# Performance work log

Hardware: AMD Instinct MI355X
Metric: run time of the kernel (lower is better)

## Reference

```python
import jax, jax.numpy as jnp
import numpy as np

N = 25000      # nodes
E = 400000     # edges
IN = 1024      # in_channels
FC = 128       # feature_channels
ADD = 20       # additional_channels
MID = (FC + ADD) // 4   # 37, fc1 output (heads=4)
OUT = 3
EPS = 1e-5
NEG_SLOPE = 0.01


def setup_inputs() -> dict:
    key = jax.random.key(0)
    ks = jax.random.split(key, 16)
    d = {}
    d["features"] = jax.random.normal(ks[0], (N, IN), dtype=jnp.float32)
    d["edges"] = jax.random.randint(ks[1], (2, E), 0, N, dtype=jnp.int64)
    d["edges2"] = jax.random.randint(ks[2], (2, 1000), 0, N, dtype=jnp.int64)
    d["edge_features"] = jax.random.normal(ks[3], (E, 1), dtype=jnp.float32)
    d["additional_feature"] = jax.random.normal(ks[4], (N, ADD), dtype=jnp.float32)
    # SAGEConv params: lin_l (neighbor path, with bias), lin_r (root path, no bias)
    s = 1.0 / np.sqrt(IN)
    d["Wl"] = jax.random.uniform(ks[5], (FC, IN), jnp.float32, -s, s)
    d["bl"] = jax.random.uniform(ks[6], (FC,), jnp.float32, -s, s)
    d["Wr"] = jax.random.uniform(ks[7], (FC, IN), jnp.float32, -s, s)
    s1 = 1.0 / np.sqrt(FC + ADD)
    d["W1"] = jax.random.uniform(ks[8], (MID, FC + ADD), jnp.float32, -s1, s1)
    d["b1"] = jax.random.uniform(ks[9], (MID,), jnp.float32, -s1, s1)
    s2 = 1.0 / np.sqrt(MID)
    d["W2"] = jax.random.uniform(ks[10], (OUT, MID), jnp.float32, -s2, s2)
    d["b2"] = jax.random.uniform(ks[11], (OUT,), jnp.float32, -s2, s2)
    # BatchNorm1d (eval mode -> running stats)
    d["gamma"] = jnp.ones((MID,), jnp.float32)
    d["beta"] = jnp.zeros((MID,), jnp.float32)
    d["run_mean"] = jax.random.normal(ks[12], (MID,), dtype=jnp.float32) * 0.1
    d["run_var"] = jnp.abs(jax.random.normal(ks[13], (MID,), dtype=jnp.float32)) * 0.1 + 1.0
    return d


def reference(features, edges, edges2, edge_features, additional_feature,
              Wl, bl, Wr, W1, b1, W2, b2, gamma, beta, run_mean, run_var):
    src, dst = edges[0], edges[1]  # PyG: messages flow source -> target
    # scatter-mean of neighbor features onto targets
    agg = jax.ops.segment_sum(features[src], dst, num_segments=N)        # [N, IN]
    deg = jax.ops.segment_sum(jnp.ones((E,), features.dtype), dst, num_segments=N)
    agg = agg / jnp.maximum(deg, 1.0)[:, None]
    # SAGEConv: lin_l(mean_neigh) + lin_r(x)
    x = agg @ Wl.T + bl + features @ Wr.T                                 # [N, FC]
    x = jnp.where(x >= 0, x, NEG_SLOPE * x)                               # leaky_relu
    # dropout is identity in eval mode
    x = jnp.concatenate([x, additional_feature], axis=1) @ W1.T + b1      # [N, MID]
    x = jnp.maximum(x, 0.0)                                               # relu
    x = gamma * (x - run_mean) * jax.lax.rsqrt(run_var + EPS) + beta      # BN eval
    return x @ W2.T + b2                                                  # [N, OUT]
```

## Files before the change

### kernel.cpp

```cpp
#include <hip/hip_runtime.h>

#define N_NODES 25000
#define N_EDGES 400000
#define IN_CH 1024
#define FC 128
#define ADD_CH 20
#define XCH 148
#define MID 37
#define OUT_CH 3
#define MAXDEG 64
#define CSTRIDE 16

typedef short bf16x8 __attribute__((ext_vector_type(8)));
typedef float f32x4 __attribute__((ext_vector_type(4)));

__device__ __forceinline__ float bflo(unsigned int v) {
    return __builtin_bit_cast(float, v << 16);
}
__device__ __forceinline__ float bfhi(unsigned int v) {
    return __builtin_bit_cast(float, v & 0xffff0000u);
}
__device__ __forceinline__ unsigned int cvtpk(float a, float b) {
    unsigned int r;
    asm("v_cvt_pk_bf16_f32 %0, %1, %2" : "=v"(r) : "v"(a), "v"(b));
    return r;
}

__device__ __forceinline__ void gload16(const void* g, void* l) {
    __builtin_amdgcn_global_load_lds(
        (const __attribute__((address_space(1))) unsigned int*)g,
        (__attribute__((address_space(3))) unsigned int*)l,
        16, 0, 0);
}

#define WSWZ_B 16
#define ZERO_B 49

__global__ __launch_bounds__(512) void prep(const float* __restrict__ Wl,
                                            const float* __restrict__ Wr,
                                            ushort* __restrict__ Wpk,
                                            int* __restrict__ cursor) {
    int b = blockIdx.x, t = threadIdx.x;
    if (b < WSWZ_B) {
        int w = t >> 6, lane = t & 63, l15 = lane & 15, q8 = (lane >> 4) * 8;
        int ch = b * 16 + l15;
        const float* src = (ch < FC) ? (Wl + (size_t)ch * IN_CH)
                                     : (Wr + (size_t)(ch - FC) * IN_CH);
        #pragma unroll
        for (int j = 0; j < 4; ++j) {
            int kt = w * 4 + j;
            float4 lo = *(const float4*)(src + kt * 32 + q8);
            float4 hi = *(const float4*)(src + kt * 32 + q8 + 4);
            uint4 pk;
            pk.x = cvtpk(lo.x, lo.y); pk.y = cvtpk(lo.z, lo.w);
            pk.z = cvtpk(hi.x, hi.y); pk.w = cvtpk(hi.z, hi.w);
            ((uint4*)Wpk)[((size_t)kt * 16 + b) * 64 + lane] = pk;
        }
    } else {
        int i = (b - WSWZ_B) * 512 + t;
        if (i < N_NODES) {
            uint4 z = {0, 0, 0, 0};
            uint4* dst = (uint4*)(cursor + (size_t)i * CSTRIDE);
            dst[0] = z; dst[1] = z; dst[2] = z; dst[3] = z;
        }
    }
}

#define GEMM_B 391
#define BUILD_B 196

__global__ __launch_bounds__(512, 4) void gemm_build(const float* __restrict__ A,
                                                     const ushort* __restrict__ Wpk,
                                                     ushort* __restrict__ Py,
                                                     ushort* __restrict__ Pz,
                                                     const int* __restrict__ edges,
                                                     int* __restrict__ cursor,
                                                     int* __restrict__ col) {
    __shared__ uint4 LDS[3][1536];
    int b = blockIdx.x, t = threadIdx.x;
    if (b >= GEMM_B) {
        int base = (b - GEMM_B) * 2048 + t;
        int src[4], dst[4], pos[4];
        #pragma unroll
        for (int k = 0; k < 4; ++k) {
            int e = base + k * 512;
            bool v = (e < N_EDGES);
            dst[k] = v ? edges[N_EDGES + e] : 0;
            src[k] = v ? edges[e] : 0;
        }
        #pragma unroll
        for (int k = 0; k < 4; ++k) {
            int e = base + k * 512;
            if (e < N_EDGES)
                pos[k] = atomicAdd(&cursor[(size_t)dst[k] * CSTRIDE], 1);
        }
        #pragma unroll
        for (int k = 0; k < 4; ++k) {
            int e = base + k * 512;
            if (e < N_EDGES && pos[k] < MAXDEG)
                col[dst[k] * MAXDEG + pos[k]] = src[k];
        }
        return;
    }
    int m0 = b * 64;

    int ga = t >> 7, hq = (t >> 6) & 1, la = t & 63;
    int nodeA = m0 + ga * 16 + (la & 15);
    if (nodeA >= N_NODES) nodeA = N_NODES - 1;
    const float* Asrc = A + (size_t)nodeA * IN_CH + (la >> 4) * 8 + hq * 4;
    const uint4* Wg = (const uint4*)Wpk;
    int tb = t & ~63;

    int w = t >> 6, lane = t & 63;
    int wm = w >> 2, wn = w & 3;
    int l15 = lane & 15, q = lane >> 4;

    f32x4 acc[4][2] = {};

    gload16(Wg + t,        &LDS[0][tb]);
    gload16(Wg + 512 + t,  &LDS[0][512 + tb]);
    gload16(Asrc,          &LDS[0][1024 + tb]);
    gload16(Wg + 1024 + t,       &LDS[1][tb]);
    gload16(Wg + 1024 + 512 + t, &LDS[1][512 + tb]);
    gload16(Asrc + 32,           &LDS[1][1024 + tb]);

    #define COMPUTE(bc)                                                           \
    {                                                                             \
        bf16x8 wf[4];                                                             \
        _Pragma("unroll")                                                         \
        for (int i = 0; i < 4; ++i)                                               \
            wf[i] = *(const bf16x8*)&LDS[bc][(wn * 4 + i) * 64 + lane];           \
        bf16x8 af[2];                                                             \
        _Pragma("unroll")                                                         \
        for (int g2 = 0; g2 < 2; ++g2) {                                          \
            f32x4 lo = *(const f32x4*)&LDS[bc][1024 + ((wm * 2 + g2) * 2 + 0) * 64 + lane]; \
            f32x4 hi = *(const f32x4*)&LDS[bc][1024 + ((wm * 2 + g2) * 2 + 1) * 64 + lane]; \
            uint4 pk;                                                             \
            pk.x = cvtpk(lo[0], lo[1]); pk.y = cvtpk(lo[2], lo[3]);               \
            pk.z = cvtpk(hi[0], hi[1]); pk.w = cvtpk(hi[2], hi[3]);               \
            af[g2] = __builtin_bit_cast(bf16x8, pk);                              \
        }                                                                         \
        _Pragma("unroll")                                                         \
        for (int i = 0; i < 4; ++i)                                               \
            _Pragma("unroll")                                                     \
            for (int g2 = 0; g2 < 2; ++g2)                                        \
                acc[i][g2] = __builtin_amdgcn_mfma_f32_16x16x32_bf16(wf[i], af[g2], acc[i][g2], 0, 0, 0); \
    }

    int bc = 0, bs = 2;
    for (int c = 0; c < 30; ++c) {
        const uint4* ws = Wg + (size_t)(c + 2) * 1024;
        gload16(ws + t,       &LDS[bs][tb]);
        gload16(ws + 512 + t, &LDS[bs][512 + tb]);
        gload16(Asrc + (size_t)(c + 2) * 32, &LDS[bs][1024 + tb]);
        asm volatile("s_waitcnt vmcnt(6)" ::: "memory");
        __builtin_amdgcn_sched_barrier(0);
        __builtin_amdgcn_s_barrier();
        __builtin_amdgcn_sched_barrier(0);
        COMPUTE(bc);
        __builtin_amdgcn_s_barrier();
        __builtin_amdgcn_sched_barrier(0);
        bc = (bc == 2) ? 0 : bc + 1;
        bs = (bs == 2) ? 0 : bs + 1;
    }
    asm volatile("s_waitcnt vmcnt(3)" ::: "memory");
    __builtin_amdgcn_sched_barrier(0);
    __builtin_amdgcn_s_barrier();
    __builtin_amdgcn_sched_barrier(0);
    COMPUTE(bc);
    bc = (bc == 2) ? 0 : bc + 1;
    asm volatile("s_waitcnt vmcnt(0)" ::: "memory");
    __builtin_amdgcn_sched_barrier(0);
    __builtin_amdgcn_s_barrier();
    __builtin_amdgcn_sched_barrier(0);
    COMPUTE(bc);
    #undef COMPUTE

    #pragma unroll
    for (int g2 = 0; g2 < 2; ++g2) {
        int node = m0 + wm * 32 + g2 * 16 + l15;
        if (node < N_NODES) {
            ushort* base = (wn < 2) ? (Py + (size_t)node * FC + (wn & 1) * 64 + q * 4)
                                    : (Pz + (size_t)node * FC + (wn & 1) * 64 + q * 4);
            #pragma unroll
            for (int i = 0; i < 4; ++i) {
                f32x4 v = acc[i][g2];
                uint2 pk;
                pk.x = cvtpk(v[0], v[1]);
                pk.y = cvtpk(v[2], v[3]);
                *(uint2*)(base + i * 16) = pk;
            }
        }
    }
}

__global__ __launch_bounds__(512) void fused_tail(const ushort* __restrict__ Py,
                                                  const ushort* __restrict__ Pz,
                                                  const int* __restrict__ deg,
                                                  const int* __restrict__ col,
                                                  const float* __restrict__ addf,
                                                  const float* __restrict__ bl,
                                                  const float* __restrict__ W1,
                                                  const float* __restrict__ b1,
                                                  const float* __restrict__ W2,
                                                  const float* __restrict__ b2,
                                                  const float* __restrict__ gamma,
                                                  const float* __restrict__ beta,
                                                  const float* __restrict__ rmean,
                                                  const float* __restrict__ rvar,
                                                  float* __restrict__ out) {
    __shared__ float W1s[XCH][MID + 3];
    __shared__ float xbuf[32][XCH + 4];
    __shared__ float hbuf[32][MID + 3];
    int t = threadIdx.x;
    for (int idx = t; idx < MID * XCH; idx += 512) {
        int j = idx / XCH, k = idx - j * XCH;
        W1s[k][j] = W1[idx];
    }
    __syncthreads();
    int w = t >> 6, lane = t & 63;
    int g = lane >> 4, c16 = lane & 15;
    #pragma unroll 1
    for (int i4 = 0; i4 < 4; ++i4) {
        int sidx = w * 4 + i4;
        int n = blockIdx.x * 32 + sidx;
        bool valid = (n < N_NODES);
        int d = valid ? deg[(size_t)n * CSTRIDE] : 0;
        if (d > MAXDEG) d = MAXDEG;
        float s[8] = {0.f, 0.f, 0.f, 0.f, 0.f, 0.f, 0.f, 0.f};
        if (d > 0) {
            int cidx = col[n * MAXDEG + (lane < d ? lane : 0)];
            for (int i = 0; i < d; i += 16) {
                int e[4];
                uint4 v[4];
                #pragma unroll
                for (int j = 0; j < 4; ++j) {
                    int ee = i + g + j * 4;
                    e[j] = __shfl(cidx, (ee < d) ? ee : 0);
                }
                #pragma unroll
                for (int j = 0; j < 4; ++j)
                    v[j] = *(const uint4*)&Py[(size_t)e[j] * FC + c16 * 8];
                #pragma unroll
                for (int j = 0; j < 4; ++j) {
                    if (i + g + j * 4 < d) {
                        s[0] += bflo(v[j].x); s[1] += bfhi(v[j].x);
                        s[2] += bflo(v[j].y); s[3] += bfhi(v[j].y);
                        s[4] += bflo(v[j].z); s[5] += bfhi(v[j].z);
                        s[6] += bflo(v[j].w); s[7] += bfhi(v[j].w);
                    }
                }
            }
            #pragma unroll
            for (int r = 0; r < 8; ++r) {
                s[r] += __shfl_xor(s[r], 16);
                s[r] += __shfl_xor(s[r], 32);
            }
        }
        if (valid) {
            if (lane < 16) {
                #pragma unroll
                for (int r = 0; r < 8; ++r) xbuf[sidx][lane * 8 + r] = s[r];
            }
            float invd = 1.0f / (float)(d > 1 ? d : 1);
            unsigned int vr = *(const unsigned int*)&Pz[(size_t)n * FC + lane * 2];
            float x0 = xbuf[sidx][2 * lane] * invd + bl[2 * lane] + bflo(vr);
            float x1 = xbuf[sidx][2 * lane + 1] * invd + bl[2 * lane + 1] + bfhi(vr);
            x0 = (x0 >= 0.f) ? x0 : 0.01f * x0;
            x1 = (x1 >= 0.f) ? x1 : 0.01f * x1;
            xbuf[sidx][2 * lane] = x0;
            xbuf[sidx][2 * lane + 1] = x1;
            if (lane < ADD_CH) xbuf[sidx][FC + lane] = addf[(size_t)n * ADD_CH + lane];
            if (lane < MID) {
                float h = b1[lane];
                #pragma unroll 4
                for (int k = 0; k < XCH; ++k) h += W1s[k][lane] * xbuf[sidx][k];
                h = fmaxf(h, 0.0f);
                h = gamma[lane] * (h - rmean[lane]) * rsqrtf(rvar[lane] + 1e-5f) + beta[lane];
                hbuf[sidx][lane] = h;
            }
            if (lane < OUT_CH) {
                float o = b2[lane];
                #pragma unroll
                for (int j = 0; j < MID; ++j) o += W2[lane * MID + j] * hbuf[sidx][j];
                out[(size_t)n * OUT_CH + lane] = o;
            }
        }
    }
}


extern "C" void kernel_launch(void* const* d_in, const int* in_sizes, int n_in,
                              void* d_out, int out_size, void* d_ws, size_t ws_size,
                              hipStream_t stream) {
    const float* features = (const float*)d_in[0];
    const int*   edges    = (const int*)d_in[1];
    const float* addf     = (const float*)d_in[4];
    const float* Wl       = (const float*)d_in[5];
    const float* bl       = (const float*)d_in[6];
    const float* Wr       = (const float*)d_in[7];
    const float* W1       = (const float*)d_in[8];
    const float* b1       = (const float*)d_in[9];
    const float* W2       = (const float*)d_in[10];
    const float* b2       = (const float*)d_in[11];
    const float* gamma    = (const float*)d_in[12];
    const float* beta     = (const float*)d_in[13];
    const float* rmean    = (const float*)d_in[14];
    const float* rvar     = (const float*)d_in[15];
    float* out = (float*)d_out;

    char* ws = (char*)d_ws;
    size_t off = 0;
    ushort* Py = (ushort*)(ws + off);     off += (size_t)N_NODES * FC * 2;
    ushort* Pz = (ushort*)(ws + off);     off += (size_t)N_NODES * FC * 2;
    ushort* Wpk = (ushort*)(ws + off);    off += (size_t)32 * 16 * 64 * 16;
    int* cursor = (int*)(ws + off);       off += (size_t)N_NODES * CSTRIDE * 4;
    int* col = (int*)(ws + off);          off += (size_t)N_NODES * MAXDEG * 4;

    prep<<<WSWZ_B + ZERO_B, 512, 0, stream>>>(Wl, Wr, Wpk, cursor);

    gemm_build<<<GEMM_B + BUILD_B, 512, 0, stream>>>(features, Wpk, Py, Pz,
                                                     edges, cursor, col);

    fused_tail<<<(N_NODES + 31) / 32, 512, 0, stream>>>(Py, Pz, cursor, col, addf, bl,
                                                        W1, b1, W2, b2, gamma, beta,
                                                        rmean, rvar, out);
}
```

Measured before the change: 273.0 us.

## Interleave neighbor gathers across four nodes per wave in fused tail

Restructures the fused_tail kernel so each wave processes its four nodes together instead of sequentially. Degree and column loads for all four nodes are issued up front, and the bf16 neighbor row gathers for all four are batched per 16-edge step. This exposes more memory-level parallelism to hide gather latency. The W1 matvec is also batched so each W1 shared-memory value is reused across four nodes. The cost is more registers per thread, with launch bounds requesting 4 waves per SIMD, which could cause spills.

```diff
diff --git a/kernel.cpp b/kernel.cpp
--- a/kernel.cpp
+++ b/kernel.cpp
@@ -194,21 +194,21 @@
     }
 }
 
-__global__ __launch_bounds__(512) void fused_tail(const ushort* __restrict__ Py,
-                                                  const ushort* __restrict__ Pz,
-                                                  const int* __restrict__ deg,
-                                                  const int* __restrict__ col,
-                                                  const float* __restrict__ addf,
-                                                  const float* __restrict__ bl,
-                                                  const float* __restrict__ W1,
-                                                  const float* __restrict__ b1,
-                                                  const float* __restrict__ W2,
-                                                  const float* __restrict__ b2,
-                                                  const float* __restrict__ gamma,
-                                                  const float* __restrict__ beta,
-                                                  const float* __restrict__ rmean,
-                                                  const float* __restrict__ rvar,
-                                                  float* __restrict__ out) {
+__global__ __launch_bounds__(512, 4) void fused_tail(const ushort* __restrict__ Py,
+                                                     const ushort* __restrict__ Pz,
+                                                     const int* __restrict__ deg,
+                                                     const int* __restrict__ col,
+                                                     const float* __restrict__ addf,
+                                                     const float* __restrict__ bl,
+                                                     const float* __restrict__ W1,
+                                                     const float* __restrict__ b1,
+                                                     const float* __restrict__ W2,
+                                                     const float* __restrict__ b2,
+                                                     const float* __restrict__ gamma,
+                                                     const float* __restrict__ beta,
+                                                     const float* __restrict__ rmean,
+                                                     const float* __restrict__ rvar,
+                                                     float* __restrict__ out) {
     __shared__ float W1s[XCH][MID + 3];
     __shared__ float xbuf[32][XCH + 4];
     __shared__ float hbuf[32][MID + 3];
@@ -220,69 +220,113 @@
     __syncthreads();
     int w = t >> 6, lane = t & 63;
     int g = lane >> 4, c16 = lane & 15;
+    int nb = blockIdx.x * 32 + w * 4;
+
+    int dd[4], cidx[4];
+    #pragma unroll
+    for (int k = 0; k < 4; ++k) {
+        int n = nb + k;
+        bool val = (n < N_NODES);
+        int d = val ? deg[(size_t)n * CSTRIDE] : 0;
+        if (d > MAXDEG) d = MAXDEG;
+        dd[k] = d;
+        cidx[k] = (val && d > 0) ? col[n * MAXDEG + (lane < d ? lane : 0)] : 0;
+    }
+
+    float s[4][8] = {};
     #pragma unroll 1
-    for (int i4 = 0; i4 < 4; ++i4) {
-        int sidx = w * 4 + i4;
-        int n = blockIdx.x * 32 + sidx;
-        bool valid = (n < N_NODES);
-        int d = valid ? deg[(size_t)n * CSTRIDE] : 0;
-        if (d > MAXDEG) d = MAXDEG;
-        float s[8] = {0.f, 0.f, 0.f, 0.f, 0.f, 0.f, 0.f, 0.f};
-        if (d > 0) {
-            int cidx = col[n * MAXDEG + (lane < d ? lane : 0)];
-            for (int i = 0; i < d; i += 16) {
-                int e[4];
-                uint4 v[4];
+    for (int it = 0; it < 4; ++it) {
+        int base = it * 16;
+        if (!((base < dd[0]) | (base < dd[1]) | (base < dd[2]) | (base < dd[3]))) break;
+        uint4 v[4][4];
+        #pragma unroll
+        for (int k = 0; k < 4; ++k) {
+            if (base < dd[k]) {
                 #pragma unroll
                 for (int j = 0; j < 4; ++j) {
-                    int ee = i + g + j * 4;
-                    e[j] = __shfl(cidx, (ee < d) ? ee : 0);
+                    int ee = base + g + j * 4;
+                    int e = __shfl(cidx[k], (ee < dd[k]) ? ee : 0);
+                    v[k][j] = *(const uint4*)&Py[(size_t)e * FC + c16 * 8];
                 }
-                #pragma unroll
-                for (int j = 0; j < 4; ++j)
-                    v[j] = *(const uint4*)&Py[(size_t)e[j] * FC + c16 * 8];
+            }
+        }
+        #pragma unroll
+        for (int k = 0; k < 4; ++k) {
+            if (base < dd[k]) {
                 #pragma unroll
                 for (int j = 0; j < 4; ++j) {
-                    if (i + g + j * 4 < d) {
-                        s[0] += bflo(v[j].x); s[1] += bfhi(v[j].x);
-                        s[2] += bflo(v[j].y); s[3] += bfhi(v[j].y);
-                        s[4] += bflo(v[j].z); s[5] += bfhi(v[j].z);
-                        s[6] += bflo(v[j].w); s[7] += bfhi(v[j].w);
+                    if (base + g + j * 4 < dd[k]) {
+                        s[k][0] += bflo(v[k][j].x); s[k][1] += bfhi(v[k][j].x);
+                        s[k][2] += bflo(v[k][j].y); s[k][3] += bfhi(v[k][j].y);
+                        s[k][4] += bflo(v[k][j].z); s[k][5] += bfhi(v[k][j].z);
+                        s[k][6] += bflo(v[k][j].w); s[k][7] += bfhi(v[k][j].w);
                     }
                 }
             }
+        }
+    }
+    #pragma unroll
+    for (int k = 0; k < 4; ++k)
+        #pragma unroll
+        for (int r = 0; r < 8; ++r) {
+            s[k][r] += __shfl_xor(s[k][r], 16);
+            s[k][r] += __shfl_xor(s[k][r], 32);
+        }
+
+    #pragma unroll
+    for (int k = 0; k < 4; ++k)
+        if (lane < 16) {
             #pragma unroll
-            for (int r = 0; r < 8; ++r) {
-                s[r] += __shfl_xor(s[r], 16);
-                s[r] += __shfl_xor(s[r], 32);
-            }
-        }
-        if (valid) {
-            if (lane < 16) {
-                #pragma unroll
-                for (int r = 0; r < 8; ++r) xbuf[sidx][lane * 8 + r] = s[r];
-            }
-            float invd = 1.0f / (float)(d > 1 ? d : 1);
-            unsigned int vr = *(const unsigned int*)&Pz[(size_t)n * FC + lane * 2];
-            float x0 = xbuf[sidx][2 * lane] * invd + bl[2 * lane] + bflo(vr);
-            float x1 = xbuf[sidx][2 * lane + 1] * invd + bl[2 * lane + 1] + bfhi(vr);
-            x0 = (x0 >= 0.f) ? x0 : 0.01f * x0;
-            x1 = (x1 >= 0.f) ? x1 : 0.01f * x1;
-            xbuf[sidx][2 * lane] = x0;
-            xbuf[sidx][2 * lane + 1] = x1;
-            if (lane < ADD_CH) xbuf[sidx][FC + lane] = addf[(size_t)n * ADD_CH + lane];
-            if (lane < MID) {
-                float h = b1[lane];
-                #pragma unroll 4
-                for (int k = 0; k < XCH; ++k) h += W1s[k][lane] * xbuf[sidx][k];
-                h = fmaxf(h, 0.0f);
-                h = gamma[lane] * (h - rmean[lane]) * rsqrtf(rvar[lane] + 1e-5f) + beta[lane];
-                hbuf[sidx][lane] = h;
-            }
-            if (lane < OUT_CH) {
+            for (int r = 0; r < 8; ++r) xbuf[w * 4 + k][lane * 8 + r] = s[k][r];
+        }
+
+    unsigned vr[4]; float afv[4];
+    #pragma unroll
+    for (int k = 0; k < 4; ++k) {
+        int n = nb + k;
+        int nc = (n < N_NODES) ? n : N_NODES - 1;
+        vr[k] = *(const unsigned*)&Pz[(size_t)nc * FC + lane * 2];
+        afv[k] = (lane < ADD_CH) ? addf[(size_t)nc * ADD_CH + lane] : 0.f;
+    }
+    #pragma unroll
+    for (int k = 0; k < 4; ++k) {
+        int sidx = w * 4 + k;
+        float invd = 1.0f / (float)(dd[k] > 1 ? dd[k] : 1);
+        float x0 = xbuf[sidx][2 * lane] * invd + bl[2 * lane] + bflo(vr[k]);
+        float x1 = xbuf[sidx][2 * lane + 1] * invd + bl[2 * lane + 1] + bfhi(vr[k]);
+        x0 = (x0 >= 0.f) ? x0 : 0.01f * x0;
+        x1 = (x1 >= 0.f) ? x1 : 0.01f * x1;
+        xbuf[sidx][2 * lane] = x0;
+        xbuf[sidx][2 * lane + 1] = x1;
+        if (lane < ADD_CH) xbuf[sidx][FC + lane] = afv[k];
+    }
+
+    if (lane < MID) {
+        float h[4] = {b1[lane], b1[lane], b1[lane], b1[lane]};
+        #pragma unroll 2
+        for (int kk = 0; kk < XCH; ++kk) {
+            float wv = W1s[kk][lane];
+            h[0] += wv * xbuf[w * 4 + 0][kk];
+            h[1] += wv * xbuf[w * 4 + 1][kk];
+            h[2] += wv * xbuf[w * 4 + 2][kk];
+            h[3] += wv * xbuf[w * 4 + 3][kk];
+        }
+        float ga_ = gamma[lane], bt = beta[lane], rm = rmean[lane];
+        float rv = rsqrtf(rvar[lane] + 1e-5f);
+        #pragma unroll
+        for (int k = 0; k < 4; ++k) {
+            float hh = fmaxf(h[k], 0.0f);
+            hbuf[w * 4 + k][lane] = ga_ * (hh - rm) * rv + bt;
+        }
+    }
+    if (lane < OUT_CH) {
+        #pragma unroll
+        for (int k = 0; k < 4; ++k) {
+            int n = nb + k;
+            if (n < N_NODES) {
                 float o = b2[lane];
                 #pragma unroll
-                for (int j = 0; j < MID; ++j) o += W2[lane * MID + j] * hbuf[sidx][j];
+                for (int j = 0; j < MID; ++j) o += W2[lane * MID + j] * hbuf[w * 4 + k][j];
                 out[(size_t)n * OUT_CH + lane] = o;
             }
         }
```

Result: faster. 261.8 us (-4.1%).
